# Optimization experiments

Hardware: AMD Instinct MI355X
Metric: run time of the kernel (lower is better)

The kernel has to match this reference:

```python
import jax, jax.numpy as jnp
import numpy as np

DIM = 64
SQRT_DIM = np.sqrt(DIM).astype(np.float32)
NEG_INF = -1e9


def setup_inputs() -> dict:
    key = jax.random.key(0)
    kq, kk, kv, km = jax.random.split(key, 4)
    B, Q, K, D = 32, 1024, 1024, DIM
    query = jax.random.normal(kq, (B, Q, D), dtype=jnp.float32)
    k = jax.random.normal(kk, (B, K, D), dtype=jnp.float32)
    value = jax.random.normal(kv, (B, K, D), dtype=jnp.float32)
    mask = jax.random.randint(km, (B, Q, K), 0, 2).astype(jnp.bool_)
    return {"query": query, "key": k, "value": value, "mask": mask}


def reference(query, key, value, mask):
    # score: [B, Q, K]
    score = jnp.einsum('bqd,bkd->bqk', query, key) / SQRT_DIM
    score = jnp.where(mask, NEG_INF, score)
    attn = jax.nn.softmax(score, axis=-1)
    context = jnp.einsum('bqk,bkd->bqd', attn, value)
    return (context, attn)
```

## Files before the change

### kernel.cpp

```cpp
#include <hip/hip_runtime.h>

constexpr int BATCH = 32;
constexpr int QLEN  = 1024;
constexpr int KLEN  = 1024;
constexpr int DIM   = 64;
constexpr int TQ    = 16;
constexpr int SC_STRIDE = 1032;
constexpr int VT_STRIDE = 136;

typedef float    f32x4 __attribute__((ext_vector_type(4)));
typedef int      i32x4 __attribute__((ext_vector_type(4)));
typedef _Float16 f16x8 __attribute__((ext_vector_type(8)));
typedef _Float16 f16x4 __attribute__((ext_vector_type(4)));

__device__ __forceinline__ f16x8 cvt_h8(f32x4 a, f32x4 b) {
  f16x8 h;
  h[0] = (_Float16)a[0]; h[1] = (_Float16)a[1]; h[2] = (_Float16)a[2]; h[3] = (_Float16)a[3];
  h[4] = (_Float16)b[0]; h[5] = (_Float16)b[1]; h[6] = (_Float16)b[2]; h[7] = (_Float16)b[3];
  return h;
}

__global__ __launch_bounds__(256, 3)
void sdpa_kernel(const float* __restrict__ Qg, const float* __restrict__ Kg,
                 const float* __restrict__ Vg, const int* __restrict__ Mg,
                 float* __restrict__ Ctx, float* __restrict__ Attn)
{
  __shared__ __attribute__((aligned(16))) _Float16 sc[TQ * SC_STRIDE];
  __shared__ __attribute__((aligned(16))) _Float16 vt[DIM * VT_STRIDE];

  const int tid  = threadIdx.x;
  const int w    = tid >> 6;
  const int l    = tid & 63;
  const int n16  = l & 15;
  const int quad = l >> 4;
  const int b    = blockIdx.y;
  const int q0   = blockIdx.x * TQ;

  const float* qbase = Qg + ((size_t)(b * QLEN + q0 + n16)) * DIM + quad * 8;
  const f16x8 aq0 = cvt_h8(*(const f32x4*)(qbase),      *(const f32x4*)(qbase + 4));
  const f16x8 aq1 = cvt_h8(*(const f32x4*)(qbase + 32), *(const f32x4*)(qbase + 36));

  #pragma unroll 4
  for (int kc = 0; kc < 16; ++kc) {
    const int col = w * 256 + kc * 16 + n16;
    const float* kbase = Kg + ((size_t)(b * KLEN + col)) * DIM + quad * 8;
    const f16x8 bk0 = cvt_h8(*(const f32x4*)(kbase),      *(const f32x4*)(kbase + 4));
    const f16x8 bk1 = cvt_h8(*(const f32x4*)(kbase + 32), *(const f32x4*)(kbase + 36));
    f32x4 acc = {0.f, 0.f, 0.f, 0.f};
    acc = __builtin_amdgcn_mfma_f32_16x16x32_f16(aq0, bk0, acc, 0, 0, 0);
    acc = __builtin_amdgcn_mfma_f32_16x16x32_f16(aq1, bk1, acc, 0, 0, 0);
    #pragma unroll
    for (int i = 0; i < 4; ++i)
      sc[(quad * 4 + i) * SC_STRIDE + col] = (_Float16)acc[i];
  }
  __syncthreads();

  for (int rr = 0; rr < 4; ++rr) {
    const int r = w * 4 + rr;
    _Float16* prow = sc + r * SC_STRIDE;
    const int* mrow = Mg + ((size_t)(b * QLEN + q0 + r)) * KLEN;
    float s[16];
    #pragma unroll
    for (int c = 0; c < 4; ++c) {
      const i32x4 mv = *(const i32x4*)(mrow + c * 256 + l * 4);
      const f16x4 hv = *(const f16x4*)(prow + c * 256 + l * 4);
      s[c * 4 + 0] = mv[0] ? -1e9f : (float)hv[0] * 0.125f;
      s[c * 4 + 1] = mv[1] ? -1e9f : (float)hv[1] * 0.125f;
      s[c * 4 + 2] = mv[2] ? -1e9f : (float)hv[2] * 0.125f;
      s[c * 4 + 3] = mv[3] ? -1e9f : (float)hv[3] * 0.125f;
    }
    float mx = s[0];
    #pragma unroll
    for (int j = 1; j < 16; ++j) mx = fmaxf(mx, s[j]);
    #pragma unroll
    for (int d = 1; d < 64; d <<= 1) mx = fmaxf(mx, __shfl_xor(mx, d, 64));
    float sum = 0.f;
    #pragma unroll
    for (int j = 0; j < 16; ++j) { s[j] = __expf(s[j] - mx); sum += s[j]; }
    #pragma unroll
    for (int d = 1; d < 64; d <<= 1) sum += __shfl_xor(sum, d, 64);
    const float inv = 1.0f / sum;
    float* arow = Attn + ((size_t)(b * QLEN + q0 + r)) * KLEN;
    #pragma unroll
    for (int c = 0; c < 4; ++c) {
      f32x4 pv = { s[c*4+0] * inv, s[c*4+1] * inv, s[c*4+2] * inv, s[c*4+3] * inv };
      *(f32x4*)(arow + c * 256 + l * 4) = pv;
      f16x4 hp = { (_Float16)pv[0], (_Float16)pv[1], (_Float16)pv[2], (_Float16)pv[3] };
      *(f16x4*)(prow + c * 256 + l * 4) = hp;
    }
  }
  __syncthreads();

  f32x4 cacc[4];
  #pragma unroll
  for (int nf = 0; nf < 4; ++nf) cacc[nf] = (f32x4){0.f, 0.f, 0.f, 0.f};

  for (int ch = 0; ch < 8; ++ch) {
    const int kb = ch * 128;
    #pragma unroll
    for (int s2 = 0; s2 < 2; ++s2) {
      const int dblk = tid & 15;
      const int kblk = (tid >> 4) + 16 * s2;
      const int k4 = kb + kblk * 4, d4 = dblk * 4;
      const float* vbase = Vg + ((size_t)(b * KLEN + k4)) * DIM + d4;
      const f32x4 r0 = *(const f32x4*)(vbase);
      const f32x4 r1 = *(const f32x4*)(vbase + 64);
      const f32x4 r2 = *(const f32x4*)(vbase + 128);
      const f32x4 r3 = *(const f32x4*)(vbase + 192);
      #pragma unroll
      for (int di = 0; di < 4; ++di) {
        f16x4 hw = { (_Float16)r0[di], (_Float16)r1[di], (_Float16)r2[di], (_Float16)r3[di] };
        *(f16x4*)(vt + (d4 + di) * VT_STRIDE + kblk * 4) = hw;
      }
    }
    __syncthreads();
    const f16x8 ap = *(const f16x8*)(sc + n16 * SC_STRIDE + kb + w * 32 + quad * 8);
    #pragma unroll
    for (int nf = 0; nf < 4; ++nf) {
      const f16x8 bv = *(const f16x8*)(vt + (nf * 16 + n16) * VT_STRIDE + w * 32 + quad * 8);
      cacc[nf] = __builtin_amdgcn_mfma_f32_16x16x32_f16(ap, bv, cacc[nf], 0, 0, 0);
    }
    __syncthreads();
  }

  float* fpart = ((float*)sc) + w * 1024;
  #pragma unroll
  for (int nf = 0; nf < 4; ++nf) {
    #pragma unroll
    for (int i = 0; i < 4; ++i)
      fpart[(quad * 4 + i) * 64 + nf * 16 + n16] = cacc[nf][i];
  }
  __syncthreads();
  {
    const float* f0 = (const float*)sc;
    const f32x4 v0 = *(const f32x4*)(f0 + tid * 4);
    const f32x4 v1 = *(const f32x4*)(f0 + 1024 + tid * 4);
    const f32x4 v2 = *(const f32x4*)(f0 + 2048 + tid * 4);
    const f32x4 v3 = *(const f32x4*)(f0 + 3072 + tid * 4);
    const f32x4 s4 = v0 + v1 + v2 + v3;
    *(f32x4*)(Ctx + ((size_t)(b * QLEN + q0)) * DIM + tid * 4) = s4;
  }
}

extern "C" void kernel_launch(void* const* d_in, const int* in_sizes, int n_in,
                              void* d_out, int out_size, void* d_ws, size_t ws_size,
                              hipStream_t stream) {
  const float* Qg = (const float*)d_in[0];
  const float* Kg = (const float*)d_in[1];
  const float* Vg = (const float*)d_in[2];
  const int*   Mg = (const int*)d_in[3];
  float* Ctx  = (float*)d_out;
  float* Attn = (float*)d_out + (size_t)BATCH * QLEN * DIM;
  dim3 grid(QLEN / TQ, BATCH);
  sdpa_kernel<<<grid, 256, 0, stream>>>(Qg, Kg, Vg, Mg, Ctx, Attn);
}
```

Before: 314.4 us.

## Pretranspose V to fp16 in a separate kernel and prefetch mask rows early

Adds a pre-pass kernel that converts V to fp16 and transposes it into workspace once per batch. The main kernel then reads it directly from global memory instead of reconverting and transposing V in shared memory for every 16-query tile. Each wave now owns 16 output columns over the full key range, which removes the cross-wave shared-memory reduction and most of the barriers. Mask loads for the first two rows are issued before the QK MFMA phase to hide their latency, and launch bounds are raised to 4 blocks per CU. The cost is an extra kernel launch, a workspace round trip, and more register pressure from the prefetched masks.

Result: no change. 312.9 us (-0.5%).

```diff
diff --git a/kernel.cpp b/kernel.cpp
--- a/kernel.cpp
+++ b/kernel.cpp
@@ -6,7 +6,6 @@
 constexpr int DIM   = 64;
 constexpr int TQ    = 16;
 constexpr int SC_STRIDE = 1032;
-constexpr int VT_STRIDE = 136;
 
 typedef float    f32x4 __attribute__((ext_vector_type(4)));
 typedef int      i32x4 __attribute__((ext_vector_type(4)));
@@ -20,13 +19,36 @@
   return h;
 }
 
-__global__ __launch_bounds__(256, 3)
+constexpr int TK = 128;
+__global__ __launch_bounds__(256)
+void vt_kernel(const float* __restrict__ V, _Float16* __restrict__ Vt) {
+  __shared__ _Float16 lt[DIM][TK + 8];
+  const int b = blockIdx.y, k0 = blockIdx.x * TK;
+  const int t = threadIdx.x;
+  const int d4 = (t & 15) * 4;
+  #pragma unroll
+  for (int p = 0; p < TK / 16; ++p) {
+    const int kl = (t >> 4) + p * 16;
+    const f32x4 v = *(const f32x4*)(V + ((size_t)(b * KLEN + k0 + kl)) * DIM + d4);
+    #pragma unroll
+    for (int j = 0; j < 4; ++j) lt[d4 + j][kl] = (_Float16)v[j];
+  }
+  __syncthreads();
+  const int d = t >> 2;
+  #pragma unroll
+  for (int j2 = 0; j2 < TK / 32; ++j2) {
+    const int seg = (t & 3) + j2 * 4;
+    *(f16x8*)(Vt + (size_t)b * DIM * KLEN + (size_t)d * KLEN + k0 + seg * 8) =
+        *(const f16x8*)(&lt[d][seg * 8]);
+  }
+}
+
+__global__ __launch_bounds__(256, 4)
 void sdpa_kernel(const float* __restrict__ Qg, const float* __restrict__ Kg,
-                 const float* __restrict__ Vg, const int* __restrict__ Mg,
+                 const _Float16* __restrict__ Vt, const int* __restrict__ Mg,
                  float* __restrict__ Ctx, float* __restrict__ Attn)
 {
   __shared__ __attribute__((aligned(16))) _Float16 sc[TQ * SC_STRIDE];
-  __shared__ __attribute__((aligned(16))) _Float16 vt[DIM * VT_STRIDE];
 
   const int tid  = threadIdx.x;
   const int w    = tid >> 6;
@@ -35,6 +57,14 @@
   const int quad = l >> 4;
   const int b    = blockIdx.y;
   const int q0   = blockIdx.x * TQ;
+
+  const int* mrow0 = Mg + ((size_t)(b * QLEN + q0 + w * 4)) * KLEN;
+  i32x4 mva[2][4];
+  #pragma unroll
+  for (int j = 0; j < 2; ++j)
+    #pragma unroll
+    for (int c = 0; c < 4; ++c)
+      mva[j][c] = *(const i32x4*)(mrow0 + j * KLEN + c * 256 + l * 4);
 
   const float* qbase = Qg + ((size_t)(b * QLEN + q0 + n16)) * DIM + quad * 8;
   const f16x8 aq0 = cvt_h8(*(const f32x4*)(qbase),      *(const f32x4*)(qbase + 4));
@@ -55,91 +85,69 @@
   }
   __syncthreads();
 
-  for (int rr = 0; rr < 4; ++rr) {
-    const int r = w * 4 + rr;
-    _Float16* prow = sc + r * SC_STRIDE;
-    const int* mrow = Mg + ((size_t)(b * QLEN + q0 + r)) * KLEN;
-    float s[16];
+  #pragma unroll
+  for (int pp = 0; pp < 2; ++pp) {
+    i32x4 mv[2][4];
+    if (pp == 0) {
+      #pragma unroll
+      for (int j = 0; j < 2; ++j)
+        #pragma unroll
+        for (int c = 0; c < 4; ++c) mv[j][c] = mva[j][c];
+    } else {
+      #pragma unroll
+      for (int j = 0; j < 2; ++j)
+        #pragma unroll
+        for (int c = 0; c < 4; ++c)
+          mv[j][c] = *(const i32x4*)(mrow0 + (2 + j) * KLEN + c * 256 + l * 4);
+    }
     #pragma unroll
-    for (int c = 0; c < 4; ++c) {
-      const i32x4 mv = *(const i32x4*)(mrow + c * 256 + l * 4);
-      const f16x4 hv = *(const f16x4*)(prow + c * 256 + l * 4);
-      s[c * 4 + 0] = mv[0] ? -1e9f : (float)hv[0] * 0.125f;
-      s[c * 4 + 1] = mv[1] ? -1e9f : (float)hv[1] * 0.125f;
-      s[c * 4 + 2] = mv[2] ? -1e9f : (float)hv[2] * 0.125f;
-      s[c * 4 + 3] = mv[3] ? -1e9f : (float)hv[3] * 0.125f;
-    }
-    float mx = s[0];
-    #pragma unroll
-    for (int j = 1; j < 16; ++j) mx = fmaxf(mx, s[j]);
-    #pragma unroll
-    for (int d = 1; d < 64; d <<= 1) mx = fmaxf(mx, __shfl_xor(mx, d, 64));
-    float sum = 0.f;
-    #pragma unroll
-    for (int j = 0; j < 16; ++j) { s[j] = __expf(s[j] - mx); sum += s[j]; }
-    #pragma unroll
-    for (int d = 1; d < 64; d <<= 1) sum += __shfl_xor(sum, d, 64);
-    const float inv = 1.0f / sum;
-    float* arow = Attn + ((size_t)(b * QLEN + q0 + r)) * KLEN;
-    #pragma unroll
-    for (int c = 0; c < 4; ++c) {
-      f32x4 pv = { s[c*4+0] * inv, s[c*4+1] * inv, s[c*4+2] * inv, s[c*4+3] * inv };
-      *(f32x4*)(arow + c * 256 + l * 4) = pv;
-      f16x4 hp = { (_Float16)pv[0], (_Float16)pv[1], (_Float16)pv[2], (_Float16)pv[3] };
-      *(f16x4*)(prow + c * 256 + l * 4) = hp;
+    for (int j = 0; j < 2; ++j) {
+      const int r = w * 4 + pp * 2 + j;
+      _Float16* prow = sc + r * SC_STRIDE;
+      float s[16];
+      #pragma unroll
+      for (int c = 0; c < 4; ++c) {
+        const f16x4 hv = *(const f16x4*)(prow + c * 256 + l * 4);
+        s[c * 4 + 0] = mv[j][c][0] ? -1e9f : (float)hv[0] * 0.125f;
+        s[c * 4 + 1] = mv[j][c][1] ? -1e9f : (float)hv[1] * 0.125f;
+        s[c * 4 + 2] = mv[j][c][2] ? -1e9f : (float)hv[2] * 0.125f;
+        s[c * 4 + 3] = mv[j][c][3] ? -1e9f : (float)hv[3] * 0.125f;
+      }
+      float mx = s[0];
+      #pragma unroll
+      for (int jj = 1; jj < 16; ++jj) mx = fmaxf(mx, s[jj]);
+      #pragma unroll
+      for (int d = 1; d < 64; d <<= 1) mx = fmaxf(mx, __shfl_xor(mx, d, 64));
+      float sum = 0.f;
+      #pragma unroll
+      for (int jj = 0; jj < 16; ++jj) { s[jj] = __expf(s[jj] - mx); sum += s[jj]; }
+      #pragma unroll
+      for (int d = 1; d < 64; d <<= 1) sum += __shfl_xor(sum, d, 64);
+      const float inv = 1.0f / sum;
+      float* arow = Attn + ((size_t)(b * QLEN + q0 + r)) * KLEN;
+      #pragma unroll
+      for (int c = 0; c < 4; ++c) {
+        f32x4 pv = { s[c*4+0] * inv, s[c*4+1] * inv, s[c*4+2] * inv, s[c*4+3] * inv };
+        *(f32x4*)(arow + c * 256 + l * 4) = pv;
+        f16x4 hp = { (_Float16)pv[0], (_Float16)pv[1], (_Float16)pv[2], (_Float16)pv[3] };
+        *(f16x4*)(prow + c * 256 + l * 4) = hp;
+      }
     }
   }
   __syncthreads();
 
-  f32x4 cacc[4];
+  const _Float16* vtb = Vt + (size_t)b * DIM * KLEN + (size_t)(w * 16 + n16) * KLEN;
+  const _Float16* prow = sc + n16 * SC_STRIDE;
+  f32x4 cacc = {0.f, 0.f, 0.f, 0.f};
+  #pragma unroll 4
+  for (int kk = 0; kk < 32; ++kk) {
+    const f16x8 ap = *(const f16x8*)(prow + kk * 32 + quad * 8);
+    const f16x8 bv = *(const f16x8*)(vtb + kk * 32 + quad * 8);
+    cacc = __builtin_amdgcn_mfma_f32_16x16x32_f16(ap, bv, cacc, 0, 0, 0);
+  }
+  float* cbase = Ctx + ((size_t)(b * QLEN + q0 + quad * 4)) * DIM + w * 16 + n16;
   #pragma unroll
-  for (int nf = 0; nf < 4; ++nf) cacc[nf] = (f32x4){0.f, 0.f, 0.f, 0.f};
-
-  for (int ch = 0; ch < 8; ++ch) {
-    const int kb = ch * 128;
-    #pragma unroll
-    for (int s2 = 0; s2 < 2; ++s2) {
-      const int dblk = tid & 15;
-      const int kblk = (tid >> 4) + 16 * s2;
-      const int k4 = kb + kblk * 4, d4 = dblk * 4;
-      const float* vbase = Vg + ((size_t)(b * KLEN + k4)) * DIM + d4;
-      const f32x4 r0 = *(const f32x4*)(vbase);
-      const f32x4 r1 = *(const f32x4*)(vbase + 64);
-      const f32x4 r2 = *(const f32x4*)(vbase + 128);
-      const f32x4 r3 = *(const f32x4*)(vbase + 192);
-      #pragma unroll
-      for (int di = 0; di < 4; ++di) {
-        f16x4 hw = { (_Float16)r0[di], (_Float16)r1[di], (_Float16)r2[di], (_Float16)r3[di] };
-        *(f16x4*)(vt + (d4 + di) * VT_STRIDE + kblk * 4) = hw;
-      }
-    }
-    __syncthreads();
-    const f16x8 ap = *(const f16x8*)(sc + n16 * SC_STRIDE + kb + w * 32 + quad * 8);
-    #pragma unroll
-    for (int nf = 0; nf < 4; ++nf) {
-      const f16x8 bv = *(const f16x8*)(vt + (nf * 16 + n16) * VT_STRIDE + w * 32 + quad * 8);
-      cacc[nf] = __builtin_amdgcn_mfma_f32_16x16x32_f16(ap, bv, cacc[nf], 0, 0, 0);
-    }
-    __syncthreads();
-  }
-
-  float* fpart = ((float*)sc) + w * 1024;
-  #pragma unroll
-  for (int nf = 0; nf < 4; ++nf) {
-    #pragma unroll
-    for (int i = 0; i < 4; ++i)
-      fpart[(quad * 4 + i) * 64 + nf * 16 + n16] = cacc[nf][i];
-  }
-  __syncthreads();
-  {
-    const float* f0 = (const float*)sc;
-    const f32x4 v0 = *(const f32x4*)(f0 + tid * 4);
-    const f32x4 v1 = *(const f32x4*)(f0 + 1024 + tid * 4);
-    const f32x4 v2 = *(const f32x4*)(f0 + 2048 + tid * 4);
-    const f32x4 v3 = *(const f32x4*)(f0 + 3072 + tid * 4);
-    const f32x4 s4 = v0 + v1 + v2 + v3;
-    *(f32x4*)(Ctx + ((size_t)(b * QLEN + q0)) * DIM + tid * 4) = s4;
-  }
+  for (int i = 0; i < 4; ++i) cbase[(size_t)i * DIM] = cacc[i];
 }
 
 extern "C" void kernel_launch(void* const* d_in, const int* in_sizes, int n_in,
@@ -151,6 +159,11 @@
   const int*   Mg = (const int*)d_in[3];
   float* Ctx  = (float*)d_out;
   float* Attn = (float*)d_out + (size_t)BATCH * QLEN * DIM;
+  _Float16* Vt = (_Float16*)d_ws;
+
+  dim3 tgrid(KLEN / TK, BATCH);
+  vt_kernel<<<tgrid, 256, 0, stream>>>(Vg, Vt);
+
   dim3 grid(QLEN / TQ, BATCH);
-  sdpa_kernel<<<grid, 256, 0, stream>>>(Qg, Kg, Vg, Mg, Ctx, Attn);
+  sdpa_kernel<<<grid, 256, 0, stream>>>(Qg, Kg, Vt, Mg, Ctx, Attn);
 }
```
